# Kernel tuning notes

Hardware: AMD Instinct MI355X
Metric: run time of the kernel (lower is better)

The kernel has to match this reference:

```python
import jax, jax.numpy as jnp
import numpy as np

L = 2048
E = 1024
H = 16
D = E // H


def setup_inputs() -> dict:
    key = jax.random.key(0)
    ks = jax.random.split(key, 9)
    inp = {
        "values": jax.random.normal(ks[0], (L, E), dtype=jnp.float32),
        "keys": jax.random.normal(ks[1], (L, E), dtype=jnp.float32),
        "query": jax.random.normal(ks[2], (L, E), dtype=jnp.float32),
        "dist_matrix": jax.random.uniform(ks[3], (L, L), dtype=jnp.float32),
        "Wv": jax.random.normal(ks[4], (E, E), dtype=jnp.float32) * 0.02,
        "Wk": jax.random.normal(ks[5], (E, E), dtype=jnp.float32) * 0.02,
        "Wq": jax.random.normal(ks[6], (E, E), dtype=jnp.float32) * 0.02,
        "Wo": jax.random.normal(ks[7], (E, E), dtype=jnp.float32) * 0.02,
        "bo": jax.random.normal(ks[8], (E,), dtype=jnp.float32) * 0.02,
    }
    return inp


def reference(values, keys, query, dist_matrix, Wv, Wk, Wq, Wo, bo):
    # Linear projections (torch Linear: x @ W.T), then split heads: [L, H, D]
    v = (values @ Wv.T).reshape(L, H, D)
    k = (keys @ Wk.T).reshape(L, H, D)
    q = (query @ Wq.T).reshape(L, H, D)

    # energy: [H, Lq, Lk]
    energy = jnp.einsum("qhd,khd->hqk", q, k)

    # distance bias: zeros -> inf, then 1/(d+1); broadcast over heads
    dm = jnp.where(dist_matrix == 0, jnp.inf, dist_matrix)
    bias = 1.0 / (dm + 1.0)
    energy = energy + bias[None, :, :]

    attn = jax.nn.softmax(energy / jnp.sqrt(jnp.float32(E)), axis=2)

    out = jnp.einsum("hql,lhd->qhd", attn, v).reshape(L, H * D)
    return out @ Wo.T + bo
```

## Files before the change

kernel.cpp:

```cpp
#include <hip/hip_runtime.h>


#define L_SEQ 2048
#define E_DIM 1024
#define H_HEADS 16
#define D_HEAD 64
#define KSPLIT 4
#define OSPLIT 2

typedef unsigned short u16;
typedef unsigned int u32;
typedef __attribute__((ext_vector_type(8))) short bf16x8;
typedef __attribute__((ext_vector_type(4))) short bf16x4;
typedef __attribute__((ext_vector_type(8))) unsigned short u16x8;
typedef __attribute__((ext_vector_type(4))) unsigned short u16x4;
typedef __attribute__((ext_vector_type(4))) float f32x4;

#define C_LOG2E_32 0.045084220027780106f

__device__ __forceinline__ float bf2f(u16 u) {
  union { u32 i; float f; } v; v.i = ((u32)u) << 16; return v.f;
}
__device__ __forceinline__ u16 f2bf(float f) {
  union { float f; u32 i; } v; v.f = f;
  u32 u = v.i;
  u += 0x7FFFu + ((u >> 16) & 1u);
  return (u16)(u >> 16);
}
__device__ __forceinline__ u32 pack_bf16_pair(float lo, float hi) {
  union { float f; u32 u; } a, b;
  a.f = lo; b.f = hi;
  return __builtin_amdgcn_perm(b.u + 0x8000u, a.u + 0x8000u, 0x07060302u);
}
__device__ __forceinline__ void gload16(const u16* g, u16* l) {
  __builtin_amdgcn_global_load_lds(
      (const __attribute__((address_space(1))) u32*)g,
      (__attribute__((address_space(3))) u32*)l, 16, 0, 0);
}

__global__ void cvt_all(const float* __restrict__ xq, const float* __restrict__ xk,
                        const float* __restrict__ xv,
                        const float* __restrict__ wq, const float* __restrict__ wk,
                        const float* __restrict__ wv, const float* __restrict__ wo,
                        const float* __restrict__ dist, const float* __restrict__ bo,
                        u16* oq, u16* ok, u16* ov,
                        u16* owq, u16* owk, u16* owv, u16* owo, u16* obias,
                        float* __restrict__ outp)
{
  size_t gid = (size_t)blockIdx.x * 256 + threadIdx.x;
  const size_t NQ = 262144;
  const size_t NW = 131072;
  const size_t DL2 = 1048576;
  const size_t FILL = DL2 + 3 * NQ + 4 * NW;

  if (gid < DL2) {
    int tile = (int)(gid >> 6);
    int ln   = (int)(gid & 63);
    int l16  = tile >> 7;
    int q16  = tile & 127;
    int qq = q16 * 16 + (ln & 15);
    int ll = l16 * 16 + (ln >> 4) * 4;
    f32x4 d4 = *(const f32x4*)&dist[(size_t)qq * L_SEQ + ll];
    u16x4 o4;
#pragma unroll
    for (int j = 0; j < 4; ++j) {
      float f = d4[j];
      f = (f == 0.f) ? 0.f : C_LOG2E_32 / (f + 1.f);
      o4[j] = f2bf(f);
    }
    *(u16x4*)&obias[(size_t)tile * 256 + ln * 4] = o4;
    return;
  }

  if (gid >= FILL) {
    size_t off = (gid - FILL) * 8;
    int n = (int)(off & (E_DIM - 1));
    *(f32x4*)&outp[off] = *(const f32x4*)&bo[n];
    *(f32x4*)&outp[off + 4] = *(const f32x4*)&bo[n + 4];
    return;
  }

  size_t g = gid - DL2;
  const float* src; u16* dst; size_t off;
  if      (g <     NQ)           { src = xq;   dst = oq;    off = g; }
  else if (g < 2 * NQ)           { src = xk;   dst = ok;    off = g - NQ; }
  else if (g < 3 * NQ)           { src = xv;   dst = ov;    off = g - 2 * NQ; }
  else if (g < 3 * NQ + NW)      { src = wq;   dst = owq;   off = g - 3 * NQ; }
  else if (g < 3 * NQ + 2 * NW)  { src = wk;   dst = owk;   off = g - 3 * NQ - NW; }
  else if (g < 3 * NQ + 3 * NW)  { src = wv;   dst = owv;   off = g - 3 * NQ - 2 * NW; }
  else                           { src = wo;   dst = owo;   off = g - 3 * NQ - 3 * NW; }

  f32x4 v0 = *(const f32x4*)&src[off * 8];
  f32x4 v1 = *(const f32x4*)&src[off * 8 + 4];
  u16x8 o;
#pragma unroll
  for (int j = 0; j < 4; ++j) {
    o[j] = f2bf(v0[j]); o[j + 4] = f2bf(v1[j]);
  }
  *(u16x8*)&dst[off * 8] = o;
}

#define TM 128
#define TN 128
#define BK 32

template<int OUTMODE>
__global__ __launch_bounds__(256, 3) void gemm_pd(
    const u16* __restrict__ A0, const u16* __restrict__ B0, void* __restrict__ C0,
    const u16* __restrict__ A1, const u16* __restrict__ B1, void* __restrict__ C1,
    const u16* __restrict__ A2, const u16* __restrict__ B2, void* __restrict__ C2,
    int M, int N, int K)
{
  const u16* A; const u16* B; void* C;
  if (OUTMODE == 2)         { A = A0; B = B0; C = C0; }
  else if (blockIdx.z == 0) { A = A0; B = B0; C = C0; }
  else if (blockIdx.z == 1) { A = A1; B = B1; C = C1; }
  else                      { A = A2; B = B2; C = C2; }

  __shared__ __align__(16) u16 As[2][TM * BK];
  __shared__ __align__(16) u16 Bs[2][TN * BK];

  const int m0 = blockIdx.y * TM;
  const int n0 = blockIdx.x * TN;
  const int t = threadIdx.x;
  const int wave = t >> 6;
  const int lane = t & 63;
  const int quad = lane >> 4;
  const int col  = lane & 15;
  const int wm = (wave >> 1) * 64;
  const int wn = (wave & 1) * 64;

  const int sr = lane >> 2;
  const int sg = ((lane & 3) ^ ((lane >> 3) & 3)) * 8;
  const u16* gA = A + (size_t)(m0 + wave * 32 + sr) * K + sg;
  const u16* gB = B + (size_t)(n0 + wave * 32 + sr) * K + sg;
  const int lo0 = (wave * 32) * BK;
  const int lo1 = (wave * 32 + 16) * BK;

  const int kbeg = (OUTMODE == 2) ? blockIdx.z * (K / OSPLIT) : 0;
  const int kend = (OUTMODE == 2) ? kbeg + K / OSPLIT : K;

  f32x4 acc[4][4];
#pragma unroll
  for (int i = 0; i < 4; ++i)
#pragma unroll
    for (int j = 0; j < 4; ++j) acc[i][j] = (f32x4){0.f, 0.f, 0.f, 0.f};

  gload16(gA + kbeg, &As[0][lo0]);
  gload16(gA + (size_t)16 * K + kbeg, &As[0][lo1]);
  gload16(gB + kbeg, &Bs[0][lo0]);
  gload16(gB + (size_t)16 * K + kbeg, &Bs[0][lo1]);

  const int slot8 = (quad ^ ((col >> 1) & 3)) * 8;

  int buf = 0;
  for (int k0 = kbeg; k0 < kend; k0 += BK) {
    __syncthreads();
    int nk = k0 + BK;
    if (nk < kend) {
      gload16(gA + nk, &As[buf ^ 1][lo0]);
      gload16(gA + (size_t)16 * K + nk, &As[buf ^ 1][lo1]);
      gload16(gB + nk, &Bs[buf ^ 1][lo0]);
      gload16(gB + (size_t)16 * K + nk, &Bs[buf ^ 1][lo1]);
    }

    bf16x8 af[4], bfr[4];
#pragma unroll
    for (int i = 0; i < 4; ++i)
      af[i] = *(const bf16x8*)&As[buf][(wm + i * 16 + col) * BK + slot8];
#pragma unroll
    for (int j = 0; j < 4; ++j)
      bfr[j] = *(const bf16x8*)&Bs[buf][(wn + j * 16 + col) * BK + slot8];

#pragma unroll
    for (int i = 0; i < 4; ++i)
#pragma unroll
      for (int j = 0; j < 4; ++j)
        acc[i][j] = __builtin_amdgcn_mfma_f32_16x16x32_bf16(af[i], bfr[j], acc[i][j], 0, 0, 0);

    buf ^= 1;
  }

  const bool transC = (OUTMODE == 0) && (blockIdx.z == 2);
#pragma unroll
  for (int i = 0; i < 4; ++i) {
    int rowb = m0 + wm + i * 16 + quad * 4;
#pragma unroll
    for (int j = 0; j < 4; ++j) {
      int cn = n0 + wn + j * 16 + col;
      if (OUTMODE == 2) {
#pragma unroll
        for (int r = 0; r < 4; ++r)
          unsafeAtomicAdd(&((float*)C)[(size_t)(rowb + r) * N + cn], acc[i][j][r]);
      } else if (transC) {
        u16x4 pk;
#pragma unroll
        for (int r = 0; r < 4; ++r) pk[r] = f2bf(acc[i][j][r]);
        *(u16x4*)&((u16*)C)[(size_t)cn * M + rowb] = pk;
      } else {
#pragma unroll
        for (int r = 0; r < 4; ++r)
          ((u16*)C)[(size_t)(rowb + r) * N + cn] = f2bf(acc[i][j][r]);
      }
    }
  }
}

#define FK 32

__global__ __launch_bounds__(256, 4) void flash8(
    const u16* __restrict__ Q, const u16* __restrict__ Kp,
    const u16* __restrict__ Vt, const u16* __restrict__ Bb,
    u16* __restrict__ Op, float* __restrict__ lp)
{
  __shared__ __align__(16) u16 Ks[2][FK * 64];
  __shared__ __align__(16) u16 Vs[2][D_HEAD * FK];

  const int h  = blockIdx.y;
  const int q0 = blockIdx.x * 128;
  const int z  = blockIdx.z;
  const int hoff = h * D_HEAD;
  const int kbase = z * (L_SEQ / KSPLIT);
  const int NT = (L_SEQ / KSPLIT) / FK;
  const int t = threadIdx.x;
  const int wave = t >> 6;
  const int lane = t & 63;
  const int quad = lane >> 4;
  const int col  = lane & 15;

  bf16x8 qf[2][2];
#pragma unroll
  for (int s = 0; s < 2; ++s) {
    const int qs = q0 + wave * 32 + s * 16;
    const u16* qrow = Q + (size_t)(qs + col) * E_DIM + hoff;
    qf[s][0] = *(const bf16x8*)(qrow + quad * 8);
    qf[s][1] = *(const bf16x8*)(qrow + 32 + quad * 8);
  }
  const int qb0 = blockIdx.x * 8 + wave * 2;
  const int lb4 = lane * 4;

  const int krow = wave * 8 + (lane >> 3);
  const int kg = ((lane & 7) ^ (lane >> 3)) * 8;
  const u16* gK = Kp + (size_t)krow * E_DIM + hoff + kg;
  const int vrow = wave * 16 + (lane >> 2);
  const int vg = ((lane & 3) ^ ((lane >> 4) & 3)) * 8;
  const u16* gV = Vt + (size_t)(hoff + vrow) * L_SEQ + vg;

  float l_lane[2] = {0.f, 0.f};
  f32x4 oacc[2][4];
#pragma unroll
  for (int s = 0; s < 2; ++s)
#pragma unroll
    for (int td = 0; td < 4; ++td) oacc[s][td] = (f32x4){0.f, 0.f, 0.f, 0.f};

  gload16(gK + (size_t)kbase * E_DIM, &Ks[0][wave * 8 * 64]);
  gload16(gV + kbase, &Vs[0][wave * 16 * FK]);
  u16x4 bv[2][2], bn[2][2];
  {
    const int kb16 = kbase >> 4;
#pragma unroll
    for (int s = 0; s < 2; ++s) {
      bv[s][0] = *(const u16x4*)&Bb[((size_t)(kb16 + 0) * 128 + qb0 + s) * 256 + lb4];
      bv[s][1] = *(const u16x4*)&Bb[((size_t)(kb16 + 1) * 128 + qb0 + s) * 256 + lb4];
    }
  }

  const int ks0 = (quad ^ (col & 7)) * 8;
  const int ks1 = ((quad + 4) ^ (col & 7)) * 8;
  const int vc2 = (col >> 2) & 3;
  const int vq1 = quad >> 1;
  const int vlo = (quad & 1) * 4;

  int buf = 0;
  for (int kt = 0; kt < NT; ++kt) {
    const int k0 = kbase + kt * FK;
    __syncthreads();
    if (kt + 1 < NT) {
      const int nk = k0 + FK;
      gload16(gK + (size_t)nk * E_DIM, &Ks[buf ^ 1][wave * 8 * 64]);
      gload16(gV + nk, &Vs[buf ^ 1][wave * 16 * FK]);
      const int nk16 = nk >> 4;
#pragma unroll
      for (int s = 0; s < 2; ++s) {
        bn[s][0] = *(const u16x4*)&Bb[((size_t)(nk16 + 0) * 128 + qb0 + s) * 256 + lb4];
        bn[s][1] = *(const u16x4*)&Bb[((size_t)(nk16 + 1) * 128 + qb0 + s) * 256 + lb4];
      }
    }
    const u16* Kb = &Ks[buf][0];
    const u16* Vb = &Vs[buf][0];

    bf16x4 vf[2][4];
#pragma unroll
    for (int tt = 0; tt < 2; ++tt) {
      const int slot = (tt * 2 + vq1) ^ vc2;
#pragma unroll
      for (int td = 0; td < 4; ++td)
        vf[tt][td] = *(const bf16x4*)&Vb[(td * 16 + col) * FK + slot * 8 + vlo];
    }

    bf16x4 pa[2][2];
#pragma unroll
    for (int tt = 0; tt < 2; ++tt) {
      const u16* kr = &Kb[(tt * 16 + col) * 64];
      bf16x8 kf0 = *(const bf16x8*)&kr[ks0];
      bf16x8 kf1 = *(const bf16x8*)&kr[ks1];
#pragma unroll
      for (int s = 0; s < 2; ++s) {
        f32x4 a = (f32x4){0.f, 0.f, 0.f, 0.f};
        a = __builtin_amdgcn_mfma_f32_16x16x32_bf16(kf0, qf[s][0], a, 0, 0, 0);
        a = __builtin_amdgcn_mfma_f32_16x16x32_bf16(kf1, qf[s][1], a, 0, 0, 0);
        float p[4];
#pragma unroll
        for (int r = 0; r < 4; ++r) {
          p[r] = __builtin_amdgcn_exp2f(fmaf(a[r], C_LOG2E_32, bf2f(bv[s][tt][r])));
          l_lane[s] += p[r];
        }
        union { u32 w[2]; bf16x4 v; } pk;
        pk.w[0] = pack_bf16_pair(p[0], p[1]);
        pk.w[1] = pack_bf16_pair(p[2], p[3]);
        pa[s][tt] = pk.v;
      }
    }

#pragma unroll
    for (int s = 0; s < 2; ++s)
#pragma unroll
      for (int td = 0; td < 4; ++td) {
        oacc[s][td] = __builtin_amdgcn_mfma_f32_16x16x16bf16_1k(
            pa[s][0], vf[0][td], oacc[s][td], 0, 0, 0);
        oacc[s][td] = __builtin_amdgcn_mfma_f32_16x16x16bf16_1k(
            pa[s][1], vf[1][td], oacc[s][td], 0, 0, 0);
      }

#pragma unroll
    for (int s = 0; s < 2; ++s) { bv[s][0] = bn[s][0]; bv[s][1] = bn[s][1]; }
    buf ^= 1;
  }

#pragma unroll
  for (int s = 0; s < 2; ++s) {
    l_lane[s] += __shfl_xor(l_lane[s], 16);
    l_lane[s] += __shfl_xor(l_lane[s], 32);
    if (lane < 16)
      lp[((size_t)z * L_SEQ + q0 + wave * 32 + s * 16 + lane) * H_HEADS + h] = l_lane[s];
  }

#pragma unroll
  for (int s = 0; s < 2; ++s) {
    const int qrow_mine = q0 + wave * 32 + s * 16 + quad * 4;
#pragma unroll
    for (int td = 0; td < 4; ++td)
#pragma unroll
      for (int r = 0; r < 4; ++r)
        Op[((size_t)z * L_SEQ + qrow_mine + r) * E_DIM + hoff + td * 16 + col] = f2bf(oacc[s][td][r]);
  }
}

__global__ void merge_attn(const u16* __restrict__ Op, const float* __restrict__ lp,
                           u16* __restrict__ AOb)
{
  size_t gid = (size_t)blockIdx.x * 256 + threadIdx.x;
  size_t idx = gid * 4;
  int q = (int)(idx >> 10);
  int e = (int)(idx & 1023);
  int h = e >> 6;
  float o[4] = {0.f, 0.f, 0.f, 0.f};
  float lsum = 0.f;
#pragma unroll
  for (int s = 0; s < KSPLIT; ++s) {
    u16x4 pv = *(const u16x4*)&Op[((size_t)s * L_SEQ + q) * E_DIM + e];
#pragma unroll
    for (int j = 0; j < 4; ++j) o[j] += bf2f(pv[j]);
    lsum += lp[((size_t)s * L_SEQ + q) * H_HEADS + h];
  }
  float inv = 1.f / lsum;
  u16x4 pk;
#pragma unroll
  for (int j = 0; j < 4; ++j) pk[j] = f2bf(o[j] * inv);
  *(u16x4*)&AOb[idx] = pk;
}

extern "C" void kernel_launch(void* const* d_in, const int* in_sizes, int n_in,
                              void* d_out, int out_size, void* d_ws, size_t ws_size,
                              hipStream_t stream)
{
  const float* values = (const float*)d_in[0];
  const float* keys   = (const float*)d_in[1];
  const float* query  = (const float*)d_in[2];
  const float* dist   = (const float*)d_in[3];
  const float* Wv     = (const float*)d_in[4];
  const float* Wk     = (const float*)d_in[5];
  const float* Wq     = (const float*)d_in[6];
  const float* Wo     = (const float*)d_in[7];
  const float* bo     = (const float*)d_in[8];
  float* out = (float*)d_out;

  const size_t MB = (size_t)1 << 20;
  char* w = (char*)d_ws;
  u16* xq  = (u16*)(w + 0 * MB);
  u16* xk  = (u16*)(w + 4 * MB);
  u16* xv  = (u16*)(w + 8 * MB);
  u16* wqb = (u16*)(w + 12 * MB);
  u16* wkb = (u16*)(w + 14 * MB);
  u16* wvb = (u16*)(w + 16 * MB);
  u16* wob = (u16*)(w + 18 * MB);
  u16* Bb  = (u16*)(w + 20 * MB);
  u16* Qh  = (u16*)(w + 28 * MB);
  u16* Kh  = (u16*)(w + 32 * MB);
  u16* Vth = (u16*)(w + 36 * MB);
  u16* AOb = (u16*)(w + 40 * MB);
  float* lp = (float*)(w + 44 * MB);
  u16* Op  = (u16*)(w + 48 * MB);

  cvt_all<<<10240, 256, 0, stream>>>(query, keys, values, Wq, Wk, Wv, Wo, dist, bo,
                                     xq, xk, xv, wqb, wkb, wvb, wob, Bb, out);

  dim3 gProj(E_DIM / TN, L_SEQ / TM, 3);
  gemm_pd<0><<<gProj, 256, 0, stream>>>(xq, wqb, Qh,
                                        xk, wkb, Kh,
                                        xv, wvb, Vth,
                                        L_SEQ, E_DIM, E_DIM);

  dim3 gAttn(L_SEQ / 128, H_HEADS, KSPLIT);
  flash8<<<gAttn, 256, 0, stream>>>(Qh, Kh, Vth, Bb, Op, lp);

  merge_attn<<<(L_SEQ * E_DIM / 4) / 256, 256, 0, stream>>>(Op, lp, AOb);

  dim3 gOut(E_DIM / TN, L_SEQ / TM, OSPLIT);
  gemm_pd<2><<<gOut, 256, 0, stream>>>(AOb, wob, out,
                                       AOb, wob, out,
                                       AOb, wob, out,
                                       L_SEQ, E_DIM, E_DIM);
}
```

Baseline: 195.9 us.

## Software-pipeline PV MFMAs one tile behind QK in flash attention

The flash attention loop is now unrolled by two with ping-pong register sets for P and V fragments. The P·V MFMAs for the previous key tile are issued alongside the QK MFMAs and exp of the current tile, with a drain step after the loop. The aim is to overlap the dependent exp/pack chain with independent matrix work and hide LDS latency for the V fragments. In exchange it holds a second set of P and V fragments in registers under a 4-waves launch bound, which risks register spills.

```diff
diff --git a/kernel.cpp b/kernel.cpp
--- a/kernel.cpp
+++ b/kernel.cpp
@@ -208,7 +208,7 @@
 
 #define FK 32
 
-__global__ __launch_bounds__(256, 4) void flash8(
+__global__ __launch_bounds__(256, 4) void flash9(
     const u16* __restrict__ Q, const u16* __restrict__ Kp,
     const u16* __restrict__ Vt, const u16* __restrict__ Bb,
     u16* __restrict__ Op, float* __restrict__ lp)
@@ -271,71 +271,90 @@
   const int vq1 = quad >> 1;
   const int vlo = (quad & 1) * 4;
 
+  bf16x4 pa0[2][2], pa1[2][2], vf0[2][4], vf1[2][4];
+
   int buf = 0;
-  for (int kt = 0; kt < NT; ++kt) {
-    const int k0 = kbase + kt * FK;
-    __syncthreads();
-    if (kt + 1 < NT) {
-      const int nk = k0 + FK;
-      gload16(gK + (size_t)nk * E_DIM, &Ks[buf ^ 1][wave * 8 * 64]);
-      gload16(gV + nk, &Vs[buf ^ 1][wave * 16 * FK]);
-      const int nk16 = nk >> 4;
-#pragma unroll
-      for (int s = 0; s < 2; ++s) {
-        bn[s][0] = *(const u16x4*)&Bb[((size_t)(nk16 + 0) * 128 + qb0 + s) * 256 + lb4];
-        bn[s][1] = *(const u16x4*)&Bb[((size_t)(nk16 + 1) * 128 + qb0 + s) * 256 + lb4];
-      }
+
+#define FSTEP(kt_, PP, VP, PC, VC)                                            \
+  {                                                                           \
+    const int k0_ = kbase + (kt_) * FK;                                       \
+    __syncthreads();               \
+    if ((kt_) + 1 < NT) {            \
+      const int nk_ = k0_ + FK;                                               \
+      gload16(gK + (size_t)nk_ * E_DIM, &Ks[buf ^ 1][wave * 8 * 64]);         \
+      gload16(gV + nk_, &Vs[buf ^ 1][wave * 16 * FK]);                        \
+      const int nk16_ = nk_ >> 4;                                             \
+      _Pragma("unroll")                                                       \
+      for (int s = 0; s < 2; ++s) {                                           \
+        bn[s][0] = *(const u16x4*)&Bb[((size_t)(nk16_ + 0) * 128 + qb0 + s) * 256 + lb4]; \
+        bn[s][1] = *(const u16x4*)&Bb[((size_t)(nk16_ + 1) * 128 + qb0 + s) * 256 + lb4]; \
+      }                                                                       \
+    }                                                                         \
+    const u16* Kb = &Ks[buf][0];                                              \
+    const u16* Vb = &Vs[buf][0];                                              \
+         \
+    if ((kt_) > 0) {                                                          \
+      _Pragma("unroll")                                                       \
+      for (int s = 0; s < 2; ++s)                                             \
+        _Pragma("unroll")                                                     \
+        for (int td = 0; td < 4; ++td) {                                      \
+          oacc[s][td] = __builtin_amdgcn_mfma_f32_16x16x16bf16_1k(            \
+              PP[s][0], VP[0][td], oacc[s][td], 0, 0, 0);                     \
+          oacc[s][td] = __builtin_amdgcn_mfma_f32_16x16x16bf16_1k(            \
+              PP[s][1], VP[1][td], oacc[s][td], 0, 0, 0);                     \
+        }                                                                     \
+    }                                                                         \
+      \
+    _Pragma("unroll")                                                         \
+    for (int tt = 0; tt < 2; ++tt) {                                          \
+      const u16* kr = &Kb[(tt * 16 + col) * 64];                              \
+      bf16x8 kf0 = *(const bf16x8*)&kr[ks0];                                  \
+      bf16x8 kf1 = *(const bf16x8*)&kr[ks1];                                  \
+      _Pragma("unroll")                                                       \
+      for (int s = 0; s < 2; ++s) {                                           \
+        f32x4 a = (f32x4){0.f, 0.f, 0.f, 0.f};                                \
+        a = __builtin_amdgcn_mfma_f32_16x16x32_bf16(kf0, qf[s][0], a, 0, 0, 0); \
+        a = __builtin_amdgcn_mfma_f32_16x16x32_bf16(kf1, qf[s][1], a, 0, 0, 0); \
+        float p[4];                                                           \
+        _Pragma("unroll")                                                     \
+        for (int r = 0; r < 4; ++r) {                                         \
+          p[r] = __builtin_amdgcn_exp2f(fmaf(a[r], C_LOG2E_32, bf2f(bv[s][tt][r]))); \
+          l_lane[s] += p[r];                                                  \
+        }                                                                     \
+        union { u32 w[2]; bf16x4 v; } pk_;                                    \
+        pk_.w[0] = pack_bf16_pair(p[0], p[1]);                                \
+        pk_.w[1] = pack_bf16_pair(p[2], p[3]);                                \
+        PC[s][tt] = pk_.v;                                                    \
+      }                                                                       \
+    }                                                                         \
+                     \
+    _Pragma("unroll")                                                         \
+    for (int tt = 0; tt < 2; ++tt) {                                          \
+      const int slot_ = (tt * 2 + vq1) ^ vc2;                                 \
+      _Pragma("unroll")                                                       \
+      for (int td = 0; td < 4; ++td)                                          \
+        VC[tt][td] = *(const bf16x4*)&Vb[(td * 16 + col) * FK + slot_ * 8 + vlo]; \
+    }                                                                         \
+    _Pragma("unroll")                                                         \
+    for (int s = 0; s < 2; ++s) { bv[s][0] = bn[s][0]; bv[s][1] = bn[s][1]; } \
+    buf ^= 1;                                                                 \
+  }
+
+  for (int kt = 0; kt < NT; kt += 2) {
+    FSTEP(kt,     pa1, vf1, pa0, vf0);
+    FSTEP(kt + 1, pa0, vf0, pa1, vf1);
+  }
+#undef FSTEP
+
+#pragma unroll
+  for (int s = 0; s < 2; ++s)
+#pragma unroll
+    for (int td = 0; td < 4; ++td) {
+      oacc[s][td] = __builtin_amdgcn_mfma_f32_16x16x16bf16_1k(
+          pa1[s][0], vf1[0][td], oacc[s][td], 0, 0, 0);
+      oacc[s][td] = __builtin_amdgcn_mfma_f32_16x16x16bf16_1k(
+          pa1[s][1], vf1[1][td], oacc[s][td], 0, 0, 0);
     }
-    const u16* Kb = &Ks[buf][0];
-    const u16* Vb = &Vs[buf][0];
-
-    bf16x4 vf[2][4];
-#pragma unroll
-    for (int tt = 0; tt < 2; ++tt) {
-      const int slot = (tt * 2 + vq1) ^ vc2;
-#pragma unroll
-      for (int td = 0; td < 4; ++td)
-        vf[tt][td] = *(const bf16x4*)&Vb[(td * 16 + col) * FK + slot * 8 + vlo];
-    }
-
-    bf16x4 pa[2][2];
-#pragma unroll
-    for (int tt = 0; tt < 2; ++tt) {
-      const u16* kr = &Kb[(tt * 16 + col) * 64];
-      bf16x8 kf0 = *(const bf16x8*)&kr[ks0];
-      bf16x8 kf1 = *(const bf16x8*)&kr[ks1];
-#pragma unroll
-      for (int s = 0; s < 2; ++s) {
-        f32x4 a = (f32x4){0.f, 0.f, 0.f, 0.f};
-        a = __builtin_amdgcn_mfma_f32_16x16x32_bf16(kf0, qf[s][0], a, 0, 0, 0);
-        a = __builtin_amdgcn_mfma_f32_16x16x32_bf16(kf1, qf[s][1], a, 0, 0, 0);
-        float p[4];
-#pragma unroll
-        for (int r = 0; r < 4; ++r) {
-          p[r] = __builtin_amdgcn_exp2f(fmaf(a[r], C_LOG2E_32, bf2f(bv[s][tt][r])));
-          l_lane[s] += p[r];
-        }
-        union { u32 w[2]; bf16x4 v; } pk;
-        pk.w[0] = pack_bf16_pair(p[0], p[1]);
-        pk.w[1] = pack_bf16_pair(p[2], p[3]);
-        pa[s][tt] = pk.v;
-      }
-    }
-
-#pragma unroll
-    for (int s = 0; s < 2; ++s)
-#pragma unroll
-      for (int td = 0; td < 4; ++td) {
-        oacc[s][td] = __builtin_amdgcn_mfma_f32_16x16x16bf16_1k(
-            pa[s][0], vf[0][td], oacc[s][td], 0, 0, 0);
-        oacc[s][td] = __builtin_amdgcn_mfma_f32_16x16x16bf16_1k(
-            pa[s][1], vf[1][td], oacc[s][td], 0, 0, 0);
-      }
-
-#pragma unroll
-    for (int s = 0; s < 2; ++s) { bv[s][0] = bn[s][0]; bv[s][1] = bn[s][1]; }
-    buf ^= 1;
-  }
 
 #pragma unroll
   for (int s = 0; s < 2; ++s) {
@@ -422,7 +441,7 @@
                                         L_SEQ, E_DIM, E_DIM);
 
   dim3 gAttn(L_SEQ / 128, H_HEADS, KSPLIT);
-  flash8<<<gAttn, 256, 0, stream>>>(Qh, Kh, Vth, Bb, Op, lp);
+  flash9<<<gAttn, 256, 0, stream>>>(Qh, Kh, Vth, Bb, Op, lp);
 
   merge_attn<<<(L_SEQ * E_DIM / 4) / 256, 256, 0, stream>>>(Op, lp, AOb);
 
```

New measurement: 197.9 us. No clear change (+1.0%).

## Halve GEMM N-tile and double K-step per barrier in GEMM and flash kernels

Applied to the files above, without the earlier changes.

The projection/output GEMM switches from 128x128 tiles with 2x2 waves to 128x64 tiles with each wave owning 32 rows, and processes 64 K-elements per barrier using two 32-wide shared sub-buffers. The flash attention kernel likewise stages two 32-key subtiles per barrier and prefetches four bias blocks at a time. The aim is fewer __syncthreads per unit of work, and for the GEMM twice as many blocks to fill the GPU. The cost is more LDS per block, which may lower occupancy, and reduced B-fragment reuse in the GEMM.

```diff
diff --git a/kernel.cpp b/kernel.cpp
--- a/kernel.cpp
+++ b/kernel.cpp
@@ -101,7 +101,7 @@
 }
 
 #define TM 128
-#define TN 128
+#define TN 64
 #define BK 32
 
 template<int OUTMODE>
@@ -117,8 +117,8 @@
   else if (blockIdx.z == 1) { A = A1; B = B1; C = C1; }
   else                      { A = A2; B = B2; C = C2; }
 
-  __shared__ __align__(16) u16 As[2][TM * BK];
-  __shared__ __align__(16) u16 Bs[2][TN * BK];
+  __shared__ __align__(16) u16 As[2][2][TM * BK];
+  __shared__ __align__(16) u16 Bs[2][2][TN * BK];
 
   const int m0 = blockIdx.y * TM;
   const int n0 = blockIdx.x * TN;
@@ -127,67 +127,75 @@
   const int lane = t & 63;
   const int quad = lane >> 4;
   const int col  = lane & 15;
-  const int wm = (wave >> 1) * 64;
-  const int wn = (wave & 1) * 64;
+  const int wm = wave * 32;
 
   const int sr = lane >> 2;
   const int sg = ((lane & 3) ^ ((lane >> 3) & 3)) * 8;
+  const int bw = wave * 16;
   const u16* gA = A + (size_t)(m0 + wave * 32 + sr) * K + sg;
-  const u16* gB = B + (size_t)(n0 + wave * 32 + sr) * K + sg;
-  const int lo0 = (wave * 32) * BK;
-  const int lo1 = (wave * 32 + 16) * BK;
+  const u16* gB = B + (size_t)(n0 + bw + sr) * K + sg;
+  const int loA0 = (wave * 32) * BK;
+  const int loA1 = (wave * 32 + 16) * BK;
+  const int loB0 = bw * BK;
 
   const int kbeg = (OUTMODE == 2) ? blockIdx.z * (K / OSPLIT) : 0;
   const int kend = (OUTMODE == 2) ? kbeg + K / OSPLIT : K;
 
-  f32x4 acc[4][4];
-#pragma unroll
-  for (int i = 0; i < 4; ++i)
+  f32x4 acc[2][4];
+#pragma unroll
+  for (int i = 0; i < 2; ++i)
 #pragma unroll
     for (int j = 0; j < 4; ++j) acc[i][j] = (f32x4){0.f, 0.f, 0.f, 0.f};
 
-  gload16(gA + kbeg, &As[0][lo0]);
-  gload16(gA + (size_t)16 * K + kbeg, &As[0][lo1]);
-  gload16(gB + kbeg, &Bs[0][lo0]);
-  gload16(gB + (size_t)16 * K + kbeg, &Bs[0][lo1]);
+#pragma unroll
+  for (int kh = 0; kh < 2; ++kh) {
+    gload16(gA + kbeg + kh * 32, &As[0][kh][loA0]);
+    gload16(gA + (size_t)16 * K + kbeg + kh * 32, &As[0][kh][loA1]);
+    gload16(gB + kbeg + kh * 32, &Bs[0][kh][loB0]);
+  }
 
   const int slot8 = (quad ^ ((col >> 1) & 3)) * 8;
 
   int buf = 0;
-  for (int k0 = kbeg; k0 < kend; k0 += BK) {
+  for (int k0 = kbeg; k0 < kend; k0 += 64) {
     __syncthreads();
-    int nk = k0 + BK;
+    int nk = k0 + 64;
     if (nk < kend) {
-      gload16(gA + nk, &As[buf ^ 1][lo0]);
-      gload16(gA + (size_t)16 * K + nk, &As[buf ^ 1][lo1]);
-      gload16(gB + nk, &Bs[buf ^ 1][lo0]);
-      gload16(gB + (size_t)16 * K + nk, &Bs[buf ^ 1][lo1]);
-    }
-
-    bf16x8 af[4], bfr[4];
-#pragma unroll
-    for (int i = 0; i < 4; ++i)
-      af[i] = *(const bf16x8*)&As[buf][(wm + i * 16 + col) * BK + slot8];
-#pragma unroll
-    for (int j = 0; j < 4; ++j)
-      bfr[j] = *(const bf16x8*)&Bs[buf][(wn + j * 16 + col) * BK + slot8];
-
-#pragma unroll
-    for (int i = 0; i < 4; ++i)
+#pragma unroll
+      for (int kh = 0; kh < 2; ++kh) {
+        gload16(gA + nk + kh * 32, &As[buf ^ 1][kh][loA0]);
+        gload16(gA + (size_t)16 * K + nk + kh * 32, &As[buf ^ 1][kh][loA1]);
+        gload16(gB + nk + kh * 32, &Bs[buf ^ 1][kh][loB0]);
+      }
+    }
+
+#pragma unroll
+    for (int kh = 0; kh < 2; ++kh) {
+      bf16x8 af[2], bfr[4];
+#pragma unroll
+      for (int i = 0; i < 2; ++i)
+        af[i] = *(const bf16x8*)&As[buf][kh][(wm + i * 16 + col) * BK + slot8];
 #pragma unroll
       for (int j = 0; j < 4; ++j)
-        acc[i][j] = __builtin_amdgcn_mfma_f32_16x16x32_bf16(af[i], bfr[j], acc[i][j], 0, 0, 0);
+        bfr[j] = *(const bf16x8*)&Bs[buf][kh][(j * 16 + col) * BK + slot8];
+
+#pragma unroll
+      for (int i = 0; i < 2; ++i)
+#pragma unroll
+        for (int j = 0; j < 4; ++j)
+          acc[i][j] = __builtin_amdgcn_mfma_f32_16x16x32_bf16(af[i], bfr[j], acc[i][j], 0, 0, 0);
+    }
 
     buf ^= 1;
   }
 
   const bool transC = (OUTMODE == 0) && (blockIdx.z == 2);
 #pragma unroll
-  for (int i = 0; i < 4; ++i) {
+  for (int i = 0; i < 2; ++i) {
     int rowb = m0 + wm + i * 16 + quad * 4;
 #pragma unroll
     for (int j = 0; j < 4; ++j) {
-      int cn = n0 + wn + j * 16 + col;
+      int cn = n0 + j * 16 + col;
       if (OUTMODE == 2) {
 #pragma unroll
         for (int r = 0; r < 4; ++r)
@@ -208,20 +216,20 @@
 
 #define FK 32
 
-__global__ __launch_bounds__(256, 4) void flash8(
+__global__ __launch_bounds__(256, 4) void flash10(
     const u16* __restrict__ Q, const u16* __restrict__ Kp,
     const u16* __restrict__ Vt, const u16* __restrict__ Bb,
     u16* __restrict__ Op, float* __restrict__ lp)
 {
-  __shared__ __align__(16) u16 Ks[2][FK * 64];
-  __shared__ __align__(16) u16 Vs[2][D_HEAD * FK];
+  __shared__ __align__(16) u16 Ks[2][2][FK * 64];
+  __shared__ __align__(16) u16 Vs[2][2][D_HEAD * FK];
 
   const int h  = blockIdx.y;
   const int q0 = blockIdx.x * 128;
   const int z  = blockIdx.z;
   const int hoff = h * D_HEAD;
   const int kbase = z * (L_SEQ / KSPLIT);
-  const int NT = (L_SEQ / KSPLIT) / FK;
+  const int NP = (L_SEQ / KSPLIT) / (2 * FK);
   const int t = threadIdx.x;
   const int wave = t >> 6;
   const int lane = t & 63;
@@ -253,16 +261,19 @@
 #pragma unroll
     for (int td = 0; td < 4; ++td) oacc[s][td] = (f32x4){0.f, 0.f, 0.f, 0.f};
 
-  gload16(gK + (size_t)kbase * E_DIM, &Ks[0][wave * 8 * 64]);
-  gload16(gV + kbase, &Vs[0][wave * 16 * FK]);
-  u16x4 bv[2][2], bn[2][2];
+#pragma unroll
+  for (int sub = 0; sub < 2; ++sub) {
+    gload16(gK + (size_t)(kbase + sub * 32) * E_DIM, &Ks[0][sub][wave * 8 * 64]);
+    gload16(gV + kbase + sub * 32, &Vs[0][sub][wave * 16 * FK]);
+  }
+  u16x4 bv[2][4], bn[2][4];
   {
     const int kb16 = kbase >> 4;
 #pragma unroll
-    for (int s = 0; s < 2; ++s) {
-      bv[s][0] = *(const u16x4*)&Bb[((size_t)(kb16 + 0) * 128 + qb0 + s) * 256 + lb4];
-      bv[s][1] = *(const u16x4*)&Bb[((size_t)(kb16 + 1) * 128 + qb0 + s) * 256 + lb4];
-    }
+    for (int s = 0; s < 2; ++s)
+#pragma unroll
+      for (int j = 0; j < 4; ++j)
+        bv[s][j] = *(const u16x4*)&Bb[((size_t)(kb16 + j) * 128 + qb0 + s) * 256 + lb4];
   }
 
   const int ks0 = (quad ^ (col & 7)) * 8;
@@ -272,68 +283,76 @@
   const int vlo = (quad & 1) * 4;
 
   int buf = 0;
-  for (int kt = 0; kt < NT; ++kt) {
-    const int k0 = kbase + kt * FK;
+  for (int kp = 0; kp < NP; ++kp) {
     __syncthreads();
-    if (kt + 1 < NT) {
-      const int nk = k0 + FK;
-      gload16(gK + (size_t)nk * E_DIM, &Ks[buf ^ 1][wave * 8 * 64]);
-      gload16(gV + nk, &Vs[buf ^ 1][wave * 16 * FK]);
+    if (kp + 1 < NP) {
+      const int nk = kbase + (kp + 1) * 64;
+#pragma unroll
+      for (int sub = 0; sub < 2; ++sub) {
+        gload16(gK + (size_t)(nk + sub * 32) * E_DIM, &Ks[buf ^ 1][sub][wave * 8 * 64]);
+        gload16(gV + nk + sub * 32, &Vs[buf ^ 1][sub][wave * 16 * FK]);
+      }
       const int nk16 = nk >> 4;
 #pragma unroll
-      for (int s = 0; s < 2; ++s) {
-        bn[s][0] = *(const u16x4*)&Bb[((size_t)(nk16 + 0) * 128 + qb0 + s) * 256 + lb4];
-        bn[s][1] = *(const u16x4*)&Bb[((size_t)(nk16 + 1) * 128 + qb0 + s) * 256 + lb4];
+      for (int s = 0; s < 2; ++s)
+#pragma unroll
+        for (int j = 0; j < 4; ++j)
+          bn[s][j] = *(const u16x4*)&Bb[((size_t)(nk16 + j) * 128 + qb0 + s) * 256 + lb4];
+    }
+
+#pragma unroll
+    for (int sub = 0; sub < 2; ++sub) {
+      const u16* Kb = &Ks[buf][sub][0];
+      const u16* Vb = &Vs[buf][sub][0];
+
+      bf16x4 vf[2][4];
+#pragma unroll
+      for (int tt = 0; tt < 2; ++tt) {
+        const int slot = (tt * 2 + vq1) ^ vc2;
+#pragma unroll
+        for (int td = 0; td < 4; ++td)
+          vf[tt][td] = *(const bf16x4*)&Vb[(td * 16 + col) * FK + slot * 8 + vlo];
       }
-    }
-    const u16* Kb = &Ks[buf][0];
-    const u16* Vb = &Vs[buf][0];
-
-    bf16x4 vf[2][4];
-#pragma unroll
-    for (int tt = 0; tt < 2; ++tt) {
-      const int slot = (tt * 2 + vq1) ^ vc2;
-#pragma unroll
-      for (int td = 0; td < 4; ++td)
-        vf[tt][td] = *(const bf16x4*)&Vb[(td * 16 + col) * FK + slot * 8 + vlo];
-    }
-
-    bf16x4 pa[2][2];
-#pragma unroll
-    for (int tt = 0; tt < 2; ++tt) {
-      const u16* kr = &Kb[(tt * 16 + col) * 64];
-      bf16x8 kf0 = *(const bf16x8*)&kr[ks0];
-      bf16x8 kf1 = *(const bf16x8*)&kr[ks1];
-#pragma unroll
-      for (int s = 0; s < 2; ++s) {
-        f32x4 a = (f32x4){0.f, 0.f, 0.f, 0.f};
-        a = __builtin_amdgcn_mfma_f32_16x16x32_bf16(kf0, qf[s][0], a, 0, 0, 0);
-        a = __builtin_amdgcn_mfma_f32_16x16x32_bf16(kf1, qf[s][1], a, 0, 0, 0);
-        float p[4];
-#pragma unroll
-        for (int r = 0; r < 4; ++r) {
-          p[r] = __builtin_amdgcn_exp2f(fmaf(a[r], C_LOG2E_32, bf2f(bv[s][tt][r])));
-          l_lane[s] += p[r];
+
+      bf16x4 pa[2][2];
+#pragma unroll
+      for (int tt = 0; tt < 2; ++tt) {
+        const u16* kr = &Kb[(tt * 16 + col) * 64];
+        bf16x8 kf0 = *(const bf16x8*)&kr[ks0];
+        bf16x8 kf1 = *(const bf16x8*)&kr[ks1];
+#pragma unroll
+        for (int s = 0; s < 2; ++s) {
+          f32x4 a = (f32x4){0.f, 0.f, 0.f, 0.f};
+          a = __builtin_amdgcn_mfma_f32_16x16x32_bf16(kf0, qf[s][0], a, 0, 0, 0);
+          a = __builtin_amdgcn_mfma_f32_16x16x32_bf16(kf1, qf[s][1], a, 0, 0, 0);
+          float p[4];
+#pragma unroll
+          for (int r = 0; r < 4; ++r) {
+            p[r] = __builtin_amdgcn_exp2f(fmaf(a[r], C_LOG2E_32, bf2f(bv[s][sub * 2 + tt][r])));
+            l_lane[s] += p[r];
+          }
+          union { u32 w[2]; bf16x4 v; } pk;
+          pk.w[0] = pack_bf16_pair(p[0], p[1]);
+          pk.w[1] = pack_bf16_pair(p[2], p[3]);
+          pa[s][tt] = pk.v;
         }
-        union { u32 w[2]; bf16x4 v; } pk;
-        pk.w[0] = pack_bf16_pair(p[0], p[1]);
-        pk.w[1] = pack_bf16_pair(p[2], p[3]);
-        pa[s][tt] = pk.v;
       }
+
+#pragma unroll
+      for (int s = 0; s < 2; ++s)
+#pragma unroll
+        for (int td = 0; td < 4; ++td) {
+          oacc[s][td] = __builtin_amdgcn_mfma_f32_16x16x16bf16_1k(
+              pa[s][0], vf[0][td], oacc[s][td], 0, 0, 0);
+          oacc[s][td] = __builtin_amdgcn_mfma_f32_16x16x16bf16_1k(
+              pa[s][1], vf[1][td], oacc[s][td], 0, 0, 0);
+        }
     }
 
 #pragma unroll
     for (int s = 0; s < 2; ++s)
 #pragma unroll
-      for (int td = 0; td < 4; ++td) {
-        oacc[s][td] = __builtin_amdgcn_mfma_f32_16x16x16bf16_1k(
-            pa[s][0], vf[0][td], oacc[s][td], 0, 0, 0);
-        oacc[s][td] = __builtin_amdgcn_mfma_f32_16x16x16bf16_1k(
-            pa[s][1], vf[1][td], oacc[s][td], 0, 0, 0);
-      }
-
-#pragma unroll
-    for (int s = 0; s < 2; ++s) { bv[s][0] = bn[s][0]; bv[s][1] = bn[s][1]; }
+      for (int j = 0; j < 4; ++j) bv[s][j] = bn[s][j];
     buf ^= 1;
   }
 
@@ -422,7 +441,7 @@
                                         L_SEQ, E_DIM, E_DIM);
 
   dim3 gAttn(L_SEQ / 128, H_HEADS, KSPLIT);
-  flash8<<<gAttn, 256, 0, stream>>>(Qh, Kh, Vth, Bb, Op, lp);
+  flash10<<<gAttn, 256, 0, stream>>>(Qh, Kh, Vth, Bb, Op, lp);
 
   merge_attn<<<(L_SEQ * E_DIM / 4) / 256, 256, 0, stream>>>(Op, lp, AOb);
 
```

After: 218.3 us. +11.4%, slower.
